# Performance work log

Measured on AMD Instinct MI355X. Metric: run time of the kernel, lower is better.

Reference implementation:

```python
import jax, jax.numpy as jnp
import numpy as np

NGRAM = 4
PAD = 0
N_LAYERS = sum(range(1, NGRAM + 1)) - 1  # 9; blocks_size = 10


def setup_inputs() -> dict:
    B, L, D, V = 8, 2048, 256, 256
    rng = np.random.default_rng(0)
    lens = rng.integers(L // 2, L + 1, size=B)
    pos = np.arange(L)
    seq = rng.integers(1, V, size=(B, L))
    seq = np.where(pos[None, :] < lens[:, None], seq, PAD)
    # per-layer block sizes: (size,offset) combos of GBST, sizes [2,2,3,3,3,4,4,4,4]
    sizes = [n for n in range(1, NGRAM + 1) for _ in range(n)][1:]
    gid = np.zeros((B, N_LAYERS, L), dtype=np.int64)
    for li, s in enumerate(sizes):
        g = pos // s + 1  # sorted contiguous group ids starting at 1
        gid[:, li, :] = np.where(pos[None, :] < lens[:, None], g[None, :], PAD)

    key = jax.random.key(0)
    ks = jax.random.split(key, 8)
    emb = jax.random.normal(ks[0], (V, D), jnp.float32) * 0.02
    conv_w = jax.random.normal(ks[1], (D, 1, NGRAM), jnp.float32) * 0.3      # depthwise Conv1d weight [out,1,k]
    conv_b = jax.random.normal(ks[2], (D,), jnp.float32) * 0.01
    proj_w = jax.random.normal(ks[3], (D, D), jnp.float32) / np.sqrt(D)      # 1x1 conv as [out,in]
    proj_b = jax.random.normal(ks[4], (D,), jnp.float32) * 0.01
    score_w = jax.random.normal(ks[5], (D,), jnp.float32) / np.sqrt(D)       # Linear(D,1)
    score_b = jnp.zeros((), jnp.float32)
    ff_w = jax.random.normal(ks[6], (D, D), jnp.float32) / np.sqrt(D)        # Linear(D,D) weight [out,in]
    ff_b = jax.random.normal(ks[7], (D,), jnp.float32) * 0.01
    return {
        "sequence": jnp.asarray(seq, jnp.int64) if jax.config.jax_enable_x64 else jnp.asarray(seq, jnp.int32),
        "group_id": jnp.asarray(gid, jnp.int64) if jax.config.jax_enable_x64 else jnp.asarray(gid, jnp.int32),
        "emb": emb, "conv_w": conv_w, "conv_b": conv_b,
        "proj_w": proj_w, "proj_b": proj_b,
        "score_w": score_w, "score_b": score_b,
        "ff_w": ff_w, "ff_b": ff_b,
    }


def _pool_one(xb, gb):
    """Per-(batch,layer) scatter_mean + broadcast back. xb:[L,D], gb:[L]."""
    L = gb.shape[0]
    mask = gb == PAD
    xm = jnp.where(mask[:, None], 0.0, xb)          # zero padded positions
    pad_g = jnp.max(gb) + 1                         # pad positions -> extra trailing group
    g = jnp.where(mask, pad_g, gb) - 1              # 0-based group ids
    sums = jax.ops.segment_sum(xm, g, num_segments=L)
    cnts = jax.ops.segment_sum(jnp.ones((L,), xb.dtype), g, num_segments=L)
    means = sums / jnp.maximum(cnts, 1.0)[:, None]
    # group ids are sorted-contiguous, so repeat_interleave(bincount) == gather
    return means[g]


def reference(sequence, group_id, emb, conv_w, conv_b, proj_w, proj_b,
              score_w, score_b, ff_w, ff_b):
    B, L = sequence.shape
    D = emb.shape[1]
    # NormalizedEmbedding: lookup * sqrt(d_model)
    x = emb[sequence] * jnp.sqrt(jnp.asarray(D, emb.dtype))          # [B,L,D]
    xp = jnp.pad(x, ((0, 0), (0, NGRAM - 1), (0, 0)))                # pad seq end
    xc = xp.transpose(0, 2, 1)                                       # [B,D,L+k-1]
    xc = jax.lax.conv_general_dilated(
        xc, conv_w, window_strides=(1,), padding='VALID',
        feature_group_count=D, dimension_numbers=('NCH', 'OIH', 'NCH'))
    xc = xc + conv_b[None, :, None]
    xc = jnp.einsum('ed,bdl->bel', proj_w, xc) + proj_b[None, :, None]
    x = xc.transpose(0, 2, 1)                                        # [B,L,D]
    seq_mask = sequence == PAD
    x = jnp.where(seq_mask[..., None], 0.0, x)

    # layers 1..9 are computed on a detached copy in the original
    xd = jax.lax.stop_gradient(x)
    pooled = jax.vmap(jax.vmap(_pool_one, in_axes=(None, 0)),
                      in_axes=(0, 0))(xd, group_id)                  # [B,9,L,D]

    block_reps = jnp.concatenate([x[:, None], pooled], axis=1)       # [B,10,L,D]
    block_reps = block_reps.transpose(0, 2, 1, 3)                    # [B,L,10,D]

    scores = jnp.einsum('blsd,d->bls', block_reps, score_w) + score_b
    blocks_mask = jnp.concatenate([sequence[:, None], group_id], axis=1)
    blocks_mask = blocks_mask.transpose(0, 2, 1) == PAD              # [B,L,10]
    neg = -jnp.finfo(scores.dtype).max
    scores = jnp.where(blocks_mask, neg, scores)
    scores = jax.nn.softmax(scores, axis=2)

    out = jnp.einsum('blsd,bls->bld', block_reps, scores)            # [B,L,D]
    out = out + jax.nn.relu(out @ ff_w.T + ff_b)
    return out
```

## Files before the change

kernel.cpp:

```cpp
#include <hip/hip_runtime.h>
#include <math.h>


#define D_ 256
#define M_ 48
#define BPB 43
#define LSTR 264

typedef __attribute__((ext_vector_type(8))) short bf16x8;
typedef __attribute__((ext_vector_type(4))) float f32x4;

__device__ __forceinline__ ushort f2bf(float f) {
    union { float f; unsigned u; } v; v.f = f;
    unsigned r = v.u + 0x7fffu + ((v.u >> 16) & 1u);
    return (ushort)(r >> 16);
}
__device__ __forceinline__ float bf2f(ushort h) {
    union { unsigned u; float f; } v; v.u = ((unsigned)h) << 16;
    return v.f;
}

#define LDB2(v0, v1, W, K8) do { \
    const ushort* bp_ = (W) + ((size_t)((K8) * 16 + w * 2) * 64 + ln) * 8; \
    v0 = *(const bf16x8*)(bp_); \
    v1 = *(const bf16x8*)(bp_ + 512); \
} while (0)

#define MFMA6(ACC, K8, v0, v1) do { \
    bf16x8 a0_ = *(const bf16x8*)&x_lds[lr][(K8) * 32 + koff]; \
    bf16x8 a1_ = *(const bf16x8*)&x_lds[16 + lr][(K8) * 32 + koff]; \
    bf16x8 a2_ = *(const bf16x8*)&x_lds[32 + lr][(K8) * 32 + koff]; \
    ACC[0][0] = __builtin_amdgcn_mfma_f32_16x16x32_bf16(a0_, v0, ACC[0][0], 0, 0, 0); \
    ACC[1][0] = __builtin_amdgcn_mfma_f32_16x16x32_bf16(a1_, v0, ACC[1][0], 0, 0, 0); \
    ACC[2][0] = __builtin_amdgcn_mfma_f32_16x16x32_bf16(a2_, v0, ACC[2][0], 0, 0, 0); \
    ACC[0][1] = __builtin_amdgcn_mfma_f32_16x16x32_bf16(a0_, v1, ACC[0][1], 0, 0, 0); \
    ACC[1][1] = __builtin_amdgcn_mfma_f32_16x16x32_bf16(a1_, v1, ACC[1][1], 0, 0, 0); \
    ACC[2][1] = __builtin_amdgcn_mfma_f32_16x16x32_bf16(a2_, v1, ACC[2][1], 0, 0, 0); \
} while (0)

#define SBAR __builtin_amdgcn_sched_barrier(0)

__global__ __launch_bounds__(256) void k_prep(
    const float* __restrict__ pw, const float* __restrict__ fw,
    ushort* __restrict__ wqp, ushort* __restrict__ wqf)
{
    int i = (blockIdx.x * 256 + threadIdx.x) * 2;
    int j  = i & 7;
    int ln = (i >> 3) & 63;
    int nb = (i >> 9) & 15;
    int k8 = i >> 13;
    int er = nb * 16 + (ln & 15);
    int k  = k8 * 32 + (ln >> 4) * 8 + j;
    float2 p2 = *(const float2*)(pw + er * D_ + k);
    float2 f2 = *(const float2*)(fw + er * D_ + k);
    ushort2 po; po.x = f2bf(p2.x); po.y = f2bf(p2.y);
    ushort2 fo; fo.x = f2bf(f2.x); fo.y = f2bf(f2.y);
    *(ushort2*)(wqp + i) = po;
    *(ushort2*)(wqf + i) = fo;
}

__global__ __launch_bounds__(512, 4) void k_main(
    const int* __restrict__ seq, const float* __restrict__ emb,
    const float* __restrict__ conv_w, const float* __restrict__ conv_b,
    const ushort* __restrict__ wqp, const float* __restrict__ proj_b,
    const float* __restrict__ score_w,
    const ushort* __restrict__ wqf, const float* __restrict__ ff_b,
    float* __restrict__ out, int L)
{
    __shared__ ushort x_lds[M_][LSTR];
    __shared__ ushort x2[M_][LSTR];
    __shared__ float xsred[8][M_];
    __shared__ float wts[8][12][4];
    const int b  = blockIdx.x / BPB;
    const int l0 = (blockIdx.x % BPB) * M_;
    const int t  = threadIdx.x;
    const int w  = t >> 6, ln = t & 63;
    const int lr = ln & 15, q = ln >> 4;
    const int koff = q * 8;
    const int g   = t >> 7;
    const int ch0 = (t & 127) * 2;
    const int base = g * 12;

    const int* seqp = seq + (size_t)b * L + l0;

    int tokv[15];
    #pragma unroll
    for (int r = 0; r < 15; ++r)
        tokv[r] = (l0 + base + r < L) ? seqp[base + r] : -1;

    unsigned long long vmask;
    {
        int sv = (ln < M_ && l0 + ln < L) ? seqp[ln] : 0;
        vmask = __ballot(sv > 0);
    }

    bf16x8 s00, s01, s10, s11, s20, s21, s30, s31;
    LDB2(s00, s01, wqp, 0);
    LDB2(s10, s11, wqp, 1);
    LDB2(s20, s21, wqp, 2);
    LDB2(s30, s31, wqp, 3);
    SBAR;

    {
        float4 wa = *(const float4*)(conv_w + ch0 * 4);
        float4 wb = *(const float4*)(conv_w + ch0 * 4 + 4);
        wa.x *= 16.f; wa.y *= 16.f; wa.z *= 16.f; wa.w *= 16.f;
        wb.x *= 16.f; wb.y *= 16.f; wb.z *= 16.f; wb.w *= 16.f;
        const float cba = conv_b[ch0], cbb = conv_b[ch0 + 1];
        float2 er[15];
        #pragma unroll
        for (int r = 0; r < 15; ++r) {
            int sn_ = __builtin_amdgcn_readfirstlane(tokv[r]);
            float2 e_; e_.x = 0.f; e_.y = 0.f;
            if (sn_ >= 0) e_ = *(const float2*)(emb + (size_t)sn_ * D_ + ch0);
            er[r] = e_;
        }
        #pragma unroll
        for (int r = 0; r < 12; ++r) {
            float cx = fmaf(wa.x, er[r].x, fmaf(wa.y, er[r+1].x,
                       fmaf(wa.z, er[r+2].x, fmaf(wa.w, er[r+3].x, cba))));
            float cy = fmaf(wb.x, er[r].y, fmaf(wb.y, er[r+1].y,
                       fmaf(wb.z, er[r+2].y, fmaf(wb.w, er[r+3].y, cbb))));
            *(unsigned*)&x_lds[base + r][ch0] =
                (unsigned)f2bf(cx) | ((unsigned)f2bf(cy) << 16);
        }
    }
    __syncthreads();

    f32x4 acc[3][2];
    #pragma unroll
    for (int s = 0; s < 3; ++s)
        #pragma unroll
        for (int n = 0; n < 2; ++n) acc[s][n] = (f32x4){0.f, 0.f, 0.f, 0.f};
    MFMA6(acc, 0, s00, s01); LDB2(s00, s01, wqp, 4); SBAR;
    MFMA6(acc, 1, s10, s11); LDB2(s10, s11, wqp, 5); SBAR;
    MFMA6(acc, 2, s20, s21); LDB2(s20, s21, wqp, 6); SBAR;
    MFMA6(acc, 3, s30, s31); LDB2(s30, s31, wqp, 7); SBAR;
    MFMA6(acc, 4, s00, s01);
    MFMA6(acc, 5, s10, s11);
    MFMA6(acc, 6, s20, s21);
    MFMA6(acc, 7, s30, s31);

    {
        float xsp[12];
        #pragma unroll
        for (int i = 0; i < 12; ++i) xsp[i] = 0.f;
        #pragma unroll
        for (int n = 0; n < 2; ++n) {
            int e = w * 32 + n * 16 + lr;
            float pb = proj_b[e], sw = score_w[e];
            #pragma unroll
            for (int s = 0; s < 3; ++s) {
                #pragma unroll
                for (int r = 0; r < 4; ++r) {
                    int row = s * 16 + q * 4 + r;
                    float v = ((vmask >> row) & 1ull) ? acc[s][n][r] + pb : 0.f;
                    x2[row][e] = f2bf(v);
                    xsp[s * 4 + r] = fmaf(v, sw, xsp[s * 4 + r]);
                }
            }
        }
        #pragma unroll
        for (int off = 1; off < 16; off <<= 1) {
            #pragma unroll
            for (int i = 0; i < 12; ++i) xsp[i] += __shfl_xor(xsp[i], off, 64);
        }
        if (lr == 0) {
            #pragma unroll
            for (int s = 0; s < 3; ++s)
                #pragma unroll
                for (int r = 0; r < 4; ++r)
                    xsred[w][s * 16 + q * 4 + r] = xsp[s * 4 + r];
        }
    }
    __syncthreads();

    LDB2(s00, s01, wqf, 0);
    LDB2(s10, s11, wqf, 1);
    LDB2(s20, s21, wqf, 2);
    LDB2(s30, s31, wqf, 3);
    SBAR;

    if (ln < 12) {
        const int p = (w >> 1) * 12 + ln;
        float xt = xsred[0][p] + xsred[1][p] + xsred[2][p] + xsred[3][p]
                 + xsred[4][p] + xsred[5][p] + xsred[6][p] + xsred[7][p];
        int i2 = ln & ~1;
        float s2 = __shfl(xt, i2, 64) + __shfl(xt, i2 + 1, 64);
        int i3 = ln - (ln % 3);
        float s3 = __shfl(xt, i3, 64) + __shfl(xt, i3 + 1, 64)
                 + __shfl(xt, i3 + 2, 64);
        int i4 = ln & ~3;
        float s4 = __shfl(xt, i4, 64) + __shfl(xt, i4 + 1, 64)
                 + __shfl(xt, i4 + 2, 64) + __shfl(xt, i4 + 3, 64);
        if (!((vmask >> p) & 1ull)) {
            wts[w][ln][0] = wts[w][ln][1] = wts[w][ln][2] = wts[w][ln][3] = 0.f;
        } else {
            int r2 = p & ~1, r4 = p & ~3;
            int r3 = p - (p % 3);
            float c2 = (float)__popcll((vmask >> r2) & 3ull);
            float c3 = (float)__popcll((vmask >> r3) & 7ull);
            float c4 = (float)__popcll((vmask >> r4) & 15ull);
            float m2 = s2 / c2, m3 = s3 / c3, m4 = s4 / c4;
            float mx = fmaxf(fmaxf(xt, m2), fmaxf(m3, m4));
            float q0 = __expf(xt - mx), q2 = __expf(m2 - mx);
            float q3 = __expf(m3 - mx), q4 = __expf(m4 - mx);
            float iZ = 1.f / (q0 + 2.f * q2 + 3.f * q3 + 4.f * q4);
            wts[w][ln][0] = q0 * iZ;
            wts[w][ln][1] = 2.f * q2 * iZ / c2;
            wts[w][ln][2] = 3.f * q3 * iZ / c3;
            wts[w][ln][3] = 4.f * q4 * iZ / c4;
        }
    }
    asm volatile("s_waitcnt lgkmcnt(0)" ::: "memory");
    SBAR;

    {
        const int r0 = g * 12;
        float2 xr[12];
        #pragma unroll
        for (int p = 0; p < 12; ++p) {
            unsigned v = *(const unsigned*)&x2[r0 + p][ch0];
            xr[p].x = bf2f((ushort)(v & 0xffff));
            xr[p].y = bf2f((ushort)(v >> 16));
        }
        float s2x[6], s2y[6], s3x[4], s3y[4], s4x[3], s4y[3];
        #pragma unroll
        for (int j = 0; j < 6; ++j) {
            s2x[j] = xr[2*j].x + xr[2*j+1].x;
            s2y[j] = xr[2*j].y + xr[2*j+1].y;
        }
        #pragma unroll
        for (int j = 0; j < 4; ++j) {
            s3x[j] = xr[3*j].x + xr[3*j+1].x + xr[3*j+2].x;
            s3y[j] = xr[3*j].y + xr[3*j+1].y + xr[3*j+2].y;
        }
        #pragma unroll
        for (int j = 0; j < 3; ++j) {
            s4x[j] = xr[4*j].x + xr[4*j+1].x + xr[4*j+2].x + xr[4*j+3].x;
            s4y[j] = xr[4*j].y + xr[4*j+1].y + xr[4*j+2].y + xr[4*j+3].y;
        }
        #pragma unroll
        for (int p = 0; p < 12; ++p) {
            float4 wv = *(const float4*)&wts[w][p][0];
            float ox = wv.x*xr[p].x + wv.y*s2x[p>>1] + wv.z*s3x[p/3] + wv.w*s4x[p>>2];
            float oy = wv.x*xr[p].y + wv.y*s2y[p>>1] + wv.z*s3y[p/3] + wv.w*s4y[p>>2];
            *(unsigned*)&x_lds[r0 + p][ch0] =
                (unsigned)f2bf(ox) | ((unsigned)f2bf(oy) << 16);
        }
    }
    __syncthreads();

    f32x4 ffa[3][2];
    #pragma unroll
    for (int s = 0; s < 3; ++s)
        #pragma unroll
        for (int n = 0; n < 2; ++n) ffa[s][n] = (f32x4){0.f, 0.f, 0.f, 0.f};
    MFMA6(ffa, 0, s00, s01); LDB2(s00, s01, wqf, 4); SBAR;
    MFMA6(ffa, 1, s10, s11); LDB2(s10, s11, wqf, 5); SBAR;
    MFMA6(ffa, 2, s20, s21); LDB2(s20, s21, wqf, 6); SBAR;
    MFMA6(ffa, 3, s30, s31); LDB2(s30, s31, wqf, 7); SBAR;
    MFMA6(ffa, 4, s00, s01);
    MFMA6(ffa, 5, s10, s11);
    MFMA6(ffa, 6, s20, s21);
    MFMA6(ffa, 7, s30, s31);

    #pragma unroll
    for (int n = 0; n < 2; ++n) {
        int e = w * 32 + n * 16 + lr;
        float fb = ff_b[e];
        #pragma unroll
        for (int s = 0; s < 3; ++s) {
            #pragma unroll
            for (int r = 0; r < 4; ++r) {
                int row = s * 16 + q * 4 + r;
                int l = l0 + row;
                if (l < L) {
                    float o = bf2f(x_lds[row][e]);
                    __builtin_nontemporal_store(
                        o + fmaxf(ffa[s][n][r] + fb, 0.f),
                        &out[((size_t)b * L + l) * D_ + e]);
                }
            }
        }
    }
}

extern "C" void kernel_launch(void* const* d_in, const int* in_sizes, int n_in,
                              void* d_out, int out_size, void* d_ws, size_t ws_size,
                              hipStream_t stream) {
    const int*   seq     = (const int*)d_in[0];
    const float* emb     = (const float*)d_in[2];
    const float* conv_w  = (const float*)d_in[3];
    const float* conv_b  = (const float*)d_in[4];
    const float* proj_w  = (const float*)d_in[5];
    const float* proj_b  = (const float*)d_in[6];
    const float* score_w = (const float*)d_in[7];
    const float* ff_w    = (const float*)d_in[9];
    const float* ff_b    = (const float*)d_in[10];
    float* out = (float*)d_out;

    const int L = 2048;
    const int B = in_sizes[0] / L;

    ushort* wqp = (ushort*)d_ws;
    ushort* wqf = wqp + D_ * D_;

    k_prep<<<D_ * D_ / 512, 256, 0, stream>>>(proj_w, ff_w, wqp, wqf);
    k_main<<<B * BPB, 512, 0, stream>>>(seq, emb, conv_w, conv_b, wqp, proj_b,
                                        score_w, wqf, ff_b, out, L);
}
```

Measured before the change: 27.72 us.

## Prefetch all weight fragments up front, keep x2 in fp32, use packed bf16 convert

All eight K-slices of both weight matrices are now loaded into registers ahead of the MFMA loops, instead of double-buffering four slices. The FF weights are issued earlier so their latency hides behind the pooling phase. The intermediate x2 buffer is stored as fp32 rather than bf16, which removes per-element conversions at the cost of more LDS. Manual bf16 rounding is replaced by the hardware v_cvt_pk_bf16_f32 instruction. Together these raise register and LDS pressure, which may reduce occupancy at launch_bounds(512,4).

```diff
diff --git a/kernel.cpp b/kernel.cpp
--- a/kernel.cpp
+++ b/kernel.cpp
@@ -6,6 +6,7 @@
 #define M_ 48
 #define BPB 43
 #define LSTR 264
+#define X2S 260
 
 typedef __attribute__((ext_vector_type(8))) short bf16x8;
 typedef __attribute__((ext_vector_type(4))) float f32x4;
@@ -18,6 +19,11 @@
 __device__ __forceinline__ float bf2f(ushort h) {
     union { unsigned u; float f; } v; v.u = ((unsigned)h) << 16;
     return v.f;
+}
+__device__ __forceinline__ unsigned cvtpk(float lo, float hi) {
+    unsigned r;
+    asm("v_cvt_pk_bf16_f32 %0, %1, %2" : "=v"(r) : "v"(lo), "v"(hi));
+    return r;
 }
 
 #define LDB2(v0, v1, W, K8) do { \
@@ -53,10 +59,8 @@
     int k  = k8 * 32 + (ln >> 4) * 8 + j;
     float2 p2 = *(const float2*)(pw + er * D_ + k);
     float2 f2 = *(const float2*)(fw + er * D_ + k);
-    ushort2 po; po.x = f2bf(p2.x); po.y = f2bf(p2.y);
-    ushort2 fo; fo.x = f2bf(f2.x); fo.y = f2bf(f2.y);
-    *(ushort2*)(wqp + i) = po;
-    *(ushort2*)(wqf + i) = fo;
+    *(unsigned*)(wqp + i) = cvtpk(p2.x, p2.y);
+    *(unsigned*)(wqf + i) = cvtpk(f2.x, f2.y);
 }
 
 __global__ __launch_bounds__(512, 4) void k_main(
@@ -68,9 +72,9 @@
     float* __restrict__ out, int L)
 {
     __shared__ ushort x_lds[M_][LSTR];
-    __shared__ ushort x2[M_][LSTR];
-    __shared__ float xsred[8][M_];
-    __shared__ float wts[8][12][4];
+    __shared__ float  x2f[M_][X2S];
+    __shared__ float  xsred[8][M_];
+    __shared__ float  wts[8][12][4];
     const int b  = blockIdx.x / BPB;
     const int l0 = (blockIdx.x % BPB) * M_;
     const int t  = threadIdx.x;
@@ -95,10 +99,15 @@
     }
 
     bf16x8 s00, s01, s10, s11, s20, s21, s30, s31;
+    bf16x8 s40, s41, s50, s51, s60, s61, s70, s71;
     LDB2(s00, s01, wqp, 0);
     LDB2(s10, s11, wqp, 1);
     LDB2(s20, s21, wqp, 2);
     LDB2(s30, s31, wqp, 3);
+    LDB2(s40, s41, wqp, 4);
+    LDB2(s50, s51, wqp, 5);
+    LDB2(s60, s61, wqp, 6);
+    LDB2(s70, s71, wqp, 7);
     SBAR;
 
     {
@@ -121,8 +130,7 @@
                        fmaf(wa.z, er[r+2].x, fmaf(wa.w, er[r+3].x, cba))));
             float cy = fmaf(wb.x, er[r].y, fmaf(wb.y, er[r+1].y,
                        fmaf(wb.z, er[r+2].y, fmaf(wb.w, er[r+3].y, cbb))));
-            *(unsigned*)&x_lds[base + r][ch0] =
-                (unsigned)f2bf(cx) | ((unsigned)f2bf(cy) << 16);
+            *(unsigned*)&x_lds[base + r][ch0] = cvtpk(cx, cy);
         }
     }
     __syncthreads();
@@ -132,14 +140,14 @@
     for (int s = 0; s < 3; ++s)
         #pragma unroll
         for (int n = 0; n < 2; ++n) acc[s][n] = (f32x4){0.f, 0.f, 0.f, 0.f};
-    MFMA6(acc, 0, s00, s01); LDB2(s00, s01, wqp, 4); SBAR;
-    MFMA6(acc, 1, s10, s11); LDB2(s10, s11, wqp, 5); SBAR;
-    MFMA6(acc, 2, s20, s21); LDB2(s20, s21, wqp, 6); SBAR;
-    MFMA6(acc, 3, s30, s31); LDB2(s30, s31, wqp, 7); SBAR;
-    MFMA6(acc, 4, s00, s01);
-    MFMA6(acc, 5, s10, s11);
-    MFMA6(acc, 6, s20, s21);
-    MFMA6(acc, 7, s30, s31);
+    MFMA6(acc, 0, s00, s01);
+    MFMA6(acc, 1, s10, s11);
+    MFMA6(acc, 2, s20, s21);
+    MFMA6(acc, 3, s30, s31);
+    MFMA6(acc, 4, s40, s41);
+    MFMA6(acc, 5, s50, s51);
+    MFMA6(acc, 6, s60, s61);
+    MFMA6(acc, 7, s70, s71);
 
     {
         float xsp[12];
@@ -155,7 +163,7 @@
                 for (int r = 0; r < 4; ++r) {
                     int row = s * 16 + q * 4 + r;
                     float v = ((vmask >> row) & 1ull) ? acc[s][n][r] + pb : 0.f;
-                    x2[row][e] = f2bf(v);
+                    x2f[row][e] = v;
                     xsp[s * 4 + r] = fmaf(v, sw, xsp[s * 4 + r]);
                 }
             }
@@ -179,6 +187,8 @@
     LDB2(s10, s11, wqf, 1);
     LDB2(s20, s21, wqf, 2);
     LDB2(s30, s31, wqf, 3);
+    LDB2(s40, s41, wqf, 4);
+    LDB2(s50, s51, wqf, 5);
     SBAR;
 
     if (ln < 12) {
@@ -219,11 +229,8 @@
         const int r0 = g * 12;
         float2 xr[12];
         #pragma unroll
-        for (int p = 0; p < 12; ++p) {
-            unsigned v = *(const unsigned*)&x2[r0 + p][ch0];
-            xr[p].x = bf2f((ushort)(v & 0xffff));
-            xr[p].y = bf2f((ushort)(v >> 16));
-        }
+        for (int p = 0; p < 12; ++p)
+            xr[p] = *(const float2*)&x2f[r0 + p][ch0];
         float s2x[6], s2y[6], s3x[4], s3y[4], s4x[3], s4y[3];
         #pragma unroll
         for (int j = 0; j < 6; ++j) {
@@ -245,10 +252,12 @@
             float4 wv = *(const float4*)&wts[w][p][0];
             float ox = wv.x*xr[p].x + wv.y*s2x[p>>1] + wv.z*s3x[p/3] + wv.w*s4x[p>>2];
             float oy = wv.x*xr[p].y + wv.y*s2y[p>>1] + wv.z*s3y[p/3] + wv.w*s4y[p>>2];
-            *(unsigned*)&x_lds[r0 + p][ch0] =
-                (unsigned)f2bf(ox) | ((unsigned)f2bf(oy) << 16);
-        }
-    }
+            *(unsigned*)&x_lds[r0 + p][ch0] = cvtpk(ox, oy);
+        }
+    }
+    LDB2(s60, s61, wqf, 6);
+    LDB2(s70, s71, wqf, 7);
+    SBAR;
     __syncthreads();
 
     f32x4 ffa[3][2];
@@ -256,14 +265,14 @@
     for (int s = 0; s < 3; ++s)
         #pragma unroll
         for (int n = 0; n < 2; ++n) ffa[s][n] = (f32x4){0.f, 0.f, 0.f, 0.f};
-    MFMA6(ffa, 0, s00, s01); LDB2(s00, s01, wqf, 4); SBAR;
-    MFMA6(ffa, 1, s10, s11); LDB2(s10, s11, wqf, 5); SBAR;
-    MFMA6(ffa, 2, s20, s21); LDB2(s20, s21, wqf, 6); SBAR;
-    MFMA6(ffa, 3, s30, s31); LDB2(s30, s31, wqf, 7); SBAR;
-    MFMA6(ffa, 4, s00, s01);
-    MFMA6(ffa, 5, s10, s11);
-    MFMA6(ffa, 6, s20, s21);
-    MFMA6(ffa, 7, s30, s31);
+    MFMA6(ffa, 0, s00, s01);
+    MFMA6(ffa, 1, s10, s11);
+    MFMA6(ffa, 2, s20, s21);
+    MFMA6(ffa, 3, s30, s31);
+    MFMA6(ffa, 4, s40, s41);
+    MFMA6(ffa, 5, s50, s51);
+    MFMA6(ffa, 6, s60, s61);
+    MFMA6(ffa, 7, s70, s71);
 
     #pragma unroll
     for (int n = 0; n < 2; ++n) {
```

After: 29.40 us. +6.1%, slower.
